# Kernel tuning notes

Measured on AMD Instinct MI355X. Metric: run time of the kernel, lower is better.

Reference implementation:

```python
import jax, jax.numpy as jnp
import numpy as np

B, N, DIM = 2, 4096, 1024
QK = 128
HID = 2048  # int(2.0 * DIM)
EPS = 1e-5


def setup_inputs() -> dict:
    key = jax.random.key(0)
    ks = jax.random.split(key, 10)
    s = lambda fan_in: 1.0 / np.sqrt(fan_in)
    return {
        "x": jax.random.normal(ks[0], (B, N, DIM), dtype=jnp.float32),
        "ln_g": jnp.ones((DIM,), jnp.float32),
        "ln_b": jnp.zeros((DIM,), jnp.float32),
        "Wh": jax.random.uniform(ks[1], (DIM, 2 * HID), jnp.float32, -s(DIM), s(DIM)),
        "bh": jax.random.uniform(ks[2], (2 * HID,), jnp.float32, -s(DIM), s(DIM)),
        "Wqk": jax.random.uniform(ks[3], (DIM, QK), jnp.float32, -s(DIM), s(DIM)),
        "bqk": jax.random.uniform(ks[4], (QK,), jnp.float32, -s(DIM), s(DIM)),
        "gamma": 1.0 + 0.02 * jax.random.normal(ks[5], (2, QK), jnp.float32),
        "beta": jnp.zeros((2, QK), jnp.float32),
        "Wo": jax.random.uniform(ks[6], (HID, DIM), jnp.float32, -s(HID), s(HID)),
        "bo": jax.random.uniform(ks[7], (DIM,), jnp.float32, -s(HID), s(HID)),
    }


def _gau(x, ln_g, ln_b, Wh, bh, Wqk, bqk, gamma, beta, Wo, bo):
    n = x.shape[-2]
    # LayerNorm
    mu = jnp.mean(x, axis=-1, keepdims=True)
    var = jnp.var(x, axis=-1, keepdims=True)
    normed = (x - mu) * jax.lax.rsqrt(var + EPS) * ln_g + ln_b
    # hidden: v and gate
    hv = jax.nn.silu(normed @ Wh + bh)           # [b, n, 2*HID]
    v, gate = hv[..., :HID], hv[..., HID:]
    # q, k via shared projection + offset-scale (2 heads)
    qk = jax.nn.silu(normed @ Wqk + bqk)         # [b, n, QK]
    q = qk * gamma[0] + beta[0]
    k = qk * gamma[1] + beta[1]
    # ReLU^2 attention, scaled by 1/seq_len
    sim = jnp.einsum('bid,bjd->bij', q, k) / n   # [b, n, n]
    attn = jnp.square(jax.nn.relu(sim))
    # causal mask (zero out strict upper triangle)
    causal = jnp.tril(jnp.ones((n, n), dtype=bool))
    attn = jnp.where(causal, attn, 0.0)
    out = jnp.einsum('bij,bjd->bid', attn, v) * gate
    out = out @ Wo + bo
    return out + x  # residual


def reference(x, ln_g, ln_b, Wh, bh, Wqk, bqk, gamma, beta, Wo, bo):
    return _gau(x, ln_g, ln_b, Wh, bh, Wqk, bqk, gamma, beta, Wo, bo)
```

## Files before the change

kernel.cpp:

```cpp
#include <hip/hip_runtime.h>
#include <math.h>

typedef unsigned short u16;
typedef unsigned int u32;
typedef __attribute__((ext_vector_type(8))) __bf16 bf16x8;
typedef __attribute__((ext_vector_type(4))) float f32x4;

#define B_ 2
#define N_ 4096
#define DIM_ 1024
#define QK_ 128
#define HID_ 2048
#define M_TOT (B_*N_)

__device__ __forceinline__ u16 f2bf(float f) {
  union { float f; u32 u; } v; v.f = f;
  u32 r = v.u + 0x7fffu + ((v.u >> 16) & 1u);
  return (u16)(r >> 16);
}
__device__ __forceinline__ float bf2f(u16 h) {
  union { u32 u; float f; } v; v.u = ((u32)h) << 16;
  return v.f;
}
__device__ __forceinline__ float silu_f(float v) { return v / (1.0f + expf(-v)); }

#define WAIT_VM(n)  asm volatile("s_waitcnt vmcnt(" #n ")" ::: "memory")
#define WAIT_LG0()  asm volatile("s_waitcnt lgkmcnt(0)" ::: "memory")

__global__ __launch_bounds__(256) void ln_kernel(
    const float* __restrict__ x, const float* __restrict__ g,
    const float* __restrict__ b, u16* __restrict__ out) {
  const int row = blockIdx.x;
  const int t = threadIdx.x;
  const float4* xr = (const float4*)(x + (size_t)row * DIM_);
  float4 v = xr[t];
  float s  = v.x + v.y + v.z + v.w;
  float s2 = v.x*v.x + v.y*v.y + v.z*v.z + v.w*v.w;
  #pragma unroll
  for (int o = 32; o > 0; o >>= 1) { s += __shfl_down(s, o); s2 += __shfl_down(s2, o); }
  __shared__ float red[2][4];
  const int wave = t >> 6, lane = t & 63;
  if (lane == 0) { red[0][wave] = s; red[1][wave] = s2; }
  __syncthreads();
  float ts  = red[0][0] + red[0][1] + red[0][2] + red[0][3];
  float ts2 = red[1][0] + red[1][1] + red[1][2] + red[1][3];
  float mu  = ts * (1.0f/(float)DIM_);
  float var = ts2 * (1.0f/(float)DIM_) - mu*mu;
  float rs  = rsqrtf(var + 1e-5f);
  const float4 gg = ((const float4*)g)[t];
  const float4 bb = ((const float4*)b)[t];
  ushort4 w;
  w.x = f2bf((v.x-mu)*rs*gg.x + bb.x);
  w.y = f2bf((v.y-mu)*rs*gg.y + bb.y);
  w.z = f2bf((v.z-mu)*rs*gg.z + bb.z);
  w.w = f2bf((v.w-mu)*rs*gg.w + bb.w);
  ((ushort4*)(out + (size_t)row*DIM_))[t] = w;
}

__global__ __launch_bounds__(256) void transpose_k(
    const float* __restrict__ in, u16* __restrict__ out, int R, int C) {
  __shared__ float tile[32][33];
  const int c0 = blockIdx.x * 32, r0 = blockIdx.y * 32;
  const int tx = threadIdx.x & 31, ty = threadIdx.x >> 5;
  #pragma unroll
  for (int i = 0; i < 4; ++i)
    tile[ty + i*8][tx] = in[(size_t)(r0 + ty + i*8) * C + c0 + tx];
  __syncthreads();
  #pragma unroll
  for (int i = 0; i < 4; ++i)
    out[(size_t)(c0 + ty + i*8) * R + r0 + tx] = f2bf(tile[tx][ty + i*8]);
}

enum { EPI_HV, EPI_QK, EPI_S, EPI_PV, EPI_O };

template<int EPI>
__global__ __launch_bounds__(256, 4) void g2(
    const u16* __restrict__ A, int lda,
    const u16* __restrict__ BT, int ldb, int K,
    void* __restrict__ Cv, int ldc,
    const float* __restrict__ f0,
    const u16* __restrict__ gateT, const float* __restrict__ xres)
{
  int bm, bn; const int bz = blockIdx.z;
  bn = blockIdx.x; bm = blockIdx.y;
  if constexpr (EPI == EPI_S) { if (bm < bn) return; }

  const u16* Ap = A; const u16* Bp = BT;
  if constexpr (EPI == EPI_S)  { Ap += (size_t)bz*N_*QK_; Bp += (size_t)bz*N_*QK_; }

  __shared__ __align__(16) u16 lds[2][128*64];
  const int tid = threadIdx.x, wave = tid >> 6, lane = tid & 63;
  const int m0 = bm*128, n0 = bn*128;
  f32x4 acc[4][4] = {};
  const int wr = (wave >> 1)*64, wc = (wave & 1)*64;

  const int srow = lane >> 3;
  const int sch  = (lane & 7) ^ srow;
  const u16* ga = Ap + (size_t)(m0 + srow)*lda + sch*8;
  const u16* gb = Bp + (size_t)(n0 + srow)*ldb + sch*8;

  const int l15   = lane & 15;
  const int cswz0 = ((((lane>>4)    ) ^ (lane&7)) << 3);
  const int cswz1 = ((((lane>>4) | 4) ^ (lane&7)) << 3);

  for (int k0 = 0; k0 < K; k0 += 64) {
    #pragma unroll
    for (int t = 0; t < 4; ++t) {
      const int chunk = wave*4 + t;
      __builtin_amdgcn_global_load_lds(
          (const __attribute__((address_space(1))) void*)(ga + (size_t)(chunk*8)*lda + k0),
          (__attribute__((address_space(3))) void*)&lds[0][chunk*512], 16, 0, 0);
      __builtin_amdgcn_global_load_lds(
          (const __attribute__((address_space(1))) void*)(gb + (size_t)(chunk*8)*ldb + k0),
          (__attribute__((address_space(3))) void*)&lds[1][chunk*512], 16, 0, 0);
    }
    __syncthreads();
    #pragma unroll
    for (int kk = 0; kk < 2; ++kk) {
      const int cs = kk ? cswz1 : cswz0;
      bf16x8 af[4], bfr[4];
      #pragma unroll
      for (int i = 0; i < 4; ++i) {
        af[i]  = *(const bf16x8*)&lds[0][(wr + i*16 + l15)*64 + cs];
        bfr[i] = *(const bf16x8*)&lds[1][(wc + i*16 + l15)*64 + cs];
      }
      #pragma unroll
      for (int i = 0; i < 4; ++i)
        #pragma unroll
        for (int j = 0; j < 4; ++j)
          acc[i][j] = __builtin_amdgcn_mfma_f32_16x16x32_bf16(af[i], bfr[j], acc[i][j], 0, 0, 0);
    }
    __syncthreads();
  }

  const int er = (lane >> 4)*4;
  #pragma unroll
  for (int i = 0; i < 4; ++i) {
    #pragma unroll
    for (int j = 0; j < 4; ++j) {
      #pragma unroll
      for (int e = 0; e < 4; ++e) {
        const int row = m0 + wr + i*16 + er + e;
        const int col = n0 + wc + j*16 + l15;
        float v = acc[i][j][e];
        if constexpr (EPI == EPI_S) {
          float p = (row >= col && v > 0.0f) ? v*v : 0.0f;
          ((u16*)Cv)[(size_t)bz*N_*N_ + (size_t)row*ldc + col] = f2bf(p);
        }
      }
    }
  }
}

template<int BM, int EPI>
__global__ __launch_bounds__(512, 2) void p8(
    const u16* __restrict__ A, int lda,
    const u16* __restrict__ BT, int ldb, int K,
    void* __restrict__ Cv, int ldc,
    const float* __restrict__ f0,
    const u16* __restrict__ gateT, const float* __restrict__ xres)
{
  constexpr int FR  = BM/32;
  constexpr int HF  = FR/2;
  constexpr int ATL = BM*64;
  constexpr int SLT = ATL + 256*64;
  __shared__ __align__(16) u16 lds[2*SLT];

  int bm, bn;
  const int bz = blockIdx.z;
  if constexpr (EPI == EPI_HV) {
    const int id  = (int)blockIdx.x + 16*(int)blockIdx.y;
    const int nid = (id & 7)*64 + (id >> 3);
    bm = nid & 15; bn = nid >> 4;
  } else if constexpr (EPI == EPI_PV) {
    bn = blockIdx.x;
    bm = bz ? ((int)gridDim.y - 1 - (int)blockIdx.y) : (int)blockIdx.y;
  } else { bm = blockIdx.x; bn = blockIdx.y; }

  const int tid = threadIdx.x, wave = tid >> 6, lane = tid & 63;
  const int wm = wave >> 2, wn = wave & 3;
  const int m0 = bm*BM, n0 = bn*256;
  const u16* Ap = A; const u16* Bp = BT;
  if constexpr (EPI == EPI_PV) { Ap += (size_t)bz*N_*N_; Bp += (size_t)bz*N_; }
  int kmax = K;
  if constexpr (EPI == EPI_PV) kmax = (bm+1)*BM;
  const int nt = kmax >> 6;

  const int l15  = lane & 15;
  const int c0   = (((lane>>4)    ) ^ (lane&7)) << 3;
  const int c1   = (((lane>>4) | 4) ^ (lane&7)) << 3;
  const int srow = lane >> 3;
  const int scol = ((lane&7) ^ (lane>>3)) << 3;

  f32x4 acc[FR][4] = {};
  bf16x8 af[HF][2], b0[2][2], b1[2][2];

  auto stage = [&](int slot, int unit, int t) {
    if (t >= nt) return;
    const int k0 = t << 6;
    if (unit == 0 || unit == 3) {
      const int ih = (unit == 3) ? 1 : 0;
      constexpr int LA = BM/128;
      #pragma unroll
      for (int l = 0; l < LA; ++l) {
        const int pa = wave*LA + l;
        const int row0 = (pa/(BM/32))*(BM/2) + ih*(BM/4) + (pa%(BM/32))*8;
        __builtin_amdgcn_global_load_lds(
          (const __attribute__((address_space(1))) void*)(Ap + (size_t)(m0+row0+srow)*lda + k0 + scol),
          (__attribute__((address_space(3))) void*)&lds[slot*SLT + row0*64], 16, 0, 0);
      }
    } else {
      const int jh = (unit == 2) ? 1 : 0;
      #pragma unroll
      for (int l = 0; l < 2; ++l) {
        const int pb = wave*2 + l;
        const int row0 = (pb>>2)*64 + jh*32 + (pb&3)*8;
        __builtin_amdgcn_global_load_lds(
          (const __attribute__((address_space(1))) void*)(Bp + (size_t)(n0+row0+srow)*ldb + k0 + scol),
          (__attribute__((address_space(3))) void*)&lds[slot*SLT + ATL + row0*64], 16, 0, 0);
      }
    }
  };
  auto rdA = [&](int slot, int ih) {
    #pragma unroll
    for (int i = 0; i < HF; ++i) {
      const int R = wm*(BM/2) + ih*(BM/4) + i*16 + l15;
      af[i][0] = *(const bf16x8*)&lds[slot*SLT + R*64 + c0];
      af[i][1] = *(const bf16x8*)&lds[slot*SLT + R*64 + c1];
    }
  };
  auto rdB = [&](int slot, int jh, bf16x8 (&bb)[2][2]) {
    #pragma unroll
    for (int j = 0; j < 2; ++j) {
      const int R = wn*64 + jh*32 + j*16 + l15;
      bb[j][0] = *(const bf16x8*)&lds[slot*SLT + ATL + R*64 + c0];
      bb[j][1] = *(const bf16x8*)&lds[slot*SLT + ATL + R*64 + c1];
    }
  };
  auto mma = [&](int ih, int jh, bf16x8 (&bb)[2][2]) {
    __builtin_amdgcn_s_setprio(1);
    #pragma unroll
    for (int i = 0; i < HF; ++i)
      #pragma unroll
      for (int j = 0; j < 2; ++j)
        #pragma unroll
        for (int kk = 0; kk < 2; ++kk)
          acc[ih*HF+i][jh*2+j] = __builtin_amdgcn_mfma_f32_16x16x32_bf16(
              af[i][kk], bb[j][kk], acc[ih*HF+i][jh*2+j], 0, 0, 0);
    __builtin_amdgcn_s_setprio(0);
  };

  #define BAR()     __builtin_amdgcn_s_barrier()
  #define PH_TAIL() { BAR(); WAIT_LG0(); }
  #define LG8()     if constexpr (BM==256) { asm volatile("s_waitcnt lgkmcnt(8)" ::: "memory"); }

  stage(0,0,0); stage(0,1,0); stage(0,2,0); stage(0,3,0);
  if constexpr (BM==256) { WAIT_VM(4); } else { WAIT_VM(3); }
  stage(1,0,1); stage(1,1,1); stage(1,2,1);
  if constexpr (BM==256) { WAIT_VM(6); } else { WAIT_VM(5); }
  BAR();

  const int iters = nt >> 1;
  for (int it = 0; it < iters; ++it) {
    const int kt = it*2;
    const bool last = (it == iters-1);
    rdA(0,0); rdB(0,0,b0); stage(1,3,kt+1);
    LG8();
    PH_TAIL(); mma(0,0,b0); BAR();
    rdB(0,1,b1); stage(0,0,kt+2);
    PH_TAIL(); mma(0,1,b1); BAR();
    rdA(0,1); stage(0,1,kt+2);
    PH_TAIL(); mma(1,1,b1); BAR();
    stage(0,2,kt+2);
    if (last) { WAIT_VM(0); }
    else if constexpr (BM==256) { WAIT_VM(6); } else { WAIT_VM(5); }
    PH_TAIL(); mma(1,0,b0); BAR();
    rdA(1,0); rdB(1,0,b0); stage(0,3,kt+2);
    LG8();
    PH_TAIL(); mma(0,0,b0); BAR();
    rdB(1,1,b1); stage(1,0,kt+3);
    PH_TAIL(); mma(0,1,b1); BAR();
    rdA(1,1); stage(1,1,kt+3);
    PH_TAIL(); mma(1,1,b1); BAR();
    stage(1,2,kt+3);
    if constexpr (BM==256) { WAIT_VM(6); } else { WAIT_VM(5); }
    PH_TAIL(); mma(1,0,b0); BAR();
  }

  const int er = (lane >> 4)*4;
  #pragma unroll
  for (int fi = 0; fi < FR; ++fi) {
    #pragma unroll
    for (int fj = 0; fj < 4; ++fj) {
      #pragma unroll
      for (int e = 0; e < 4; ++e) {
        const int row = m0 + wm*(BM/2) + fi*16 + er + e;
        const int col = n0 + wn*64 + fj*16 + l15;
        float v = acc[fi][fj][e];
        if constexpr (EPI == EPI_HV) {
          ((u16*)Cv)[(size_t)row*ldc + col] = f2bf(silu_f(v + f0[row]));
        } else if constexpr (EPI == EPI_PV) {
          float gate = bf2f(gateT[(size_t)(HID_ + col)*M_TOT + (size_t)bz*N_ + row]);
          ((u16*)Cv)[((size_t)bz*N_ + row)*ldc + col] = f2bf(v * gate);
        } else {
          ((float*)Cv)[(size_t)row*ldc + col] = v + f0[col] + xres[(size_t)row*DIM_ + col];
        }
      }
    }
  }
  #undef BAR
  #undef PH_TAIL
  #undef LG8
}

template<int BM, int EPI>
__global__ __launch_bounds__(256, 2) void ring4(
    const u16* __restrict__ A, int lda,
    const u16* __restrict__ BT, int ldb, int K,
    void* __restrict__ Cv, void* __restrict__ C2v, int ldc,
    const float* __restrict__ f0, const float* __restrict__ f1,
    const float* __restrict__ f2)
{
  constexpr int FRM  = BM/32;
  constexpr int LA   = BM/64;
  constexpr int ASZ  = BM*32;
  constexpr int SLOT = ASZ + 128*32;
  __shared__ __align__(16) u16 lds[4*SLOT];

  const int bm = blockIdx.x, bn = blockIdx.y;
  const int tid = threadIdx.x, wave = tid >> 6, lane = tid & 63;
  const int wm = wave >> 1, wn = wave & 1;
  const int m0 = bm*BM, n0 = bn*128;
  const int nt = K >> 5;

  f32x4 acc[FRM][4] = {};
  const int srow = lane >> 2;
  const int sq   = (lane & 3) ^ ((srow >> 1) & 3);

  auto stage = [&](int t) {
    if (t >= nt) return;
    const int k0 = t << 5;
    u16* sA = &lds[(t & 3) * SLOT];
    u16* sB = sA + ASZ;
    #pragma unroll
    for (int c = 0; c < LA; ++c) {
      const int ch = wave*LA + c;
      const u16* src = A + (size_t)(m0 + ch*16 + srow)*lda + k0 + sq*8;
      __builtin_amdgcn_global_load_lds(
          (const __attribute__((address_space(1))) void*)src,
          (__attribute__((address_space(3))) void*)(sA + ch*512), 16, 0, 0);
    }
    #pragma unroll
    for (int c = 0; c < 2; ++c) {
      const int ch = wave*2 + c;
      const u16* src = BT + (size_t)(n0 + ch*16 + srow)*ldb + k0 + sq*8;
      __builtin_amdgcn_global_load_lds(
          (const __attribute__((address_space(1))) void*)src,
          (__attribute__((address_space(3))) void*)(sB + ch*512), 16, 0, 0);
    }
  };

  stage(0); stage(1); stage(2);

  const int l15 = lane & 15;
  const int swz = (((lane >> 4) ^ ((l15 >> 1) & 3)) << 3);
  const int rA0 = (wm*(BM/2) + l15)*32;
  const int rB0 = (wn*64 + l15)*32;

  for (int t = 0; t < nt; ++t) {
    if (t + 2 < nt)      { WAIT_VM(8); }
    else if (t + 1 < nt) { WAIT_VM(4); }
    else                 { WAIT_VM(0); }
    __builtin_amdgcn_s_barrier();
    stage(t + 3);

    const u16* sA = &lds[(t & 3) * SLOT];
    const u16* sB = sA + ASZ;
    bf16x8 a_[FRM], b_[4];
    #pragma unroll
    for (int j = 0; j < 4; ++j) b_[j] = *(const bf16x8*)&sB[rB0 + j*512 + swz];
    #pragma unroll
    for (int i = 0; i < FRM; ++i) a_[i] = *(const bf16x8*)&sA[rA0 + i*512 + swz];
    #pragma unroll
    for (int i = 0; i < FRM; ++i)
      #pragma unroll
      for (int j = 0; j < 4; ++j)
        acc[i][j] = __builtin_amdgcn_mfma_f32_16x16x32_bf16(a_[i], b_[j], acc[i][j], 0, 0, 0);
  }

  const int er = (lane >> 4)*4;
  #pragma unroll
  for (int fi = 0; fi < FRM; ++fi) {
    #pragma unroll
    for (int fj = 0; fj < 4; ++fj) {
      #pragma unroll
      for (int e = 0; e < 4; ++e) {
        const int row = m0 + wm*(BM/2) + fi*16 + er + e;
        const int col = n0 + wn*64 + fj*16 + l15;
        float v = acc[fi][fj][e];
        if constexpr (EPI == EPI_QK) {
          float s = silu_f(v + f0[col]);
          float q = (s*f1[col]     + f2[col])     * (1.0f/(float)N_);
          float k2 = s*f1[QK_+col] + f2[QK_+col];
          ((u16*)Cv )[(size_t)row*ldc + col] = f2bf(q);
          ((u16*)C2v)[(size_t)row*ldc + col] = f2bf(k2);
        }
      }
    }
  }
}

extern "C" void kernel_launch(void* const* d_in, const int* in_sizes, int n_in,
                              void* d_out, int out_size, void* d_ws, size_t ws_size,
                              hipStream_t stream) {
  const float* x    = (const float*)d_in[0];
  const float* ln_g = (const float*)d_in[1];
  const float* ln_b = (const float*)d_in[2];
  const float* Wh   = (const float*)d_in[3];
  const float* bh   = (const float*)d_in[4];
  const float* Wqk  = (const float*)d_in[5];
  const float* bqk  = (const float*)d_in[6];
  const float* gamma= (const float*)d_in[7];
  const float* beta = (const float*)d_in[8];
  const float* Wo   = (const float*)d_in[9];
  const float* bo   = (const float*)d_in[10];
  float* out = (float*)d_out;
  char* ws = (char*)d_ws;

  u16* normed = (u16*)(ws + 0);
  u16* WhT    = (u16*)(ws + 16777216);
  u16* WqkT   = (u16*)(ws + 25165824);
  u16* WoT    = (u16*)(ws + 25427968);
  u16* hvT    = (u16*)(ws + 29622272);
  u16* qs     = (u16*)(ws + 96731136);
  u16* kb     = (u16*)(ws + 98828288);
  u16* P      = (u16*)(ws + 100925440);
  u16* a2     = (u16*)(ws + 168034304);

  ln_kernel<<<M_TOT, 256, 0, stream>>>(x, ln_g, ln_b, normed);
  transpose_k<<<dim3(4096/32, 1024/32), 256, 0, stream>>>(Wh,  WhT,  1024, 4096);
  transpose_k<<<dim3( 128/32, 1024/32), 256, 0, stream>>>(Wqk, WqkT, 1024, 128);
  transpose_k<<<dim3(1024/32, 2048/32), 256, 0, stream>>>(Wo,  WoT,  2048, 1024);

  p8<256, EPI_HV><<<dim3(16, 32), 512, 0, stream>>>(WhT, 1024, normed, 1024, 1024,
      hvT, 8192, bh, nullptr, nullptr);
  ring4<64, EPI_QK><<<dim3(128, 1), 256, 0, stream>>>(normed, 1024, WqkT, 1024, 1024,
      qs, kb, 128, bqk, gamma, beta);
  g2<EPI_S><<<dim3(32, 32, 2), 256, 0, stream>>>(qs, 128, kb, 128, 128,
      P, 4096, nullptr, nullptr, nullptr);
  p8<128, EPI_PV><<<dim3(8, 32, 2), 512, 0, stream>>>(P, 4096, hvT, 8192, 4096,
      a2, 2048, nullptr, hvT, nullptr);
  p8<128, EPI_O><<<dim3(64, 4), 512, 0, stream>>>(a2, 2048, WoT, 2048, 2048,
      out, 1024, bo, nullptr, x);
}
```

Baseline: 266.4 us.

## Swap GEMM kernels: HV projection on g2 tiles, score GEMM on ring4 pipeline

The hidden projection GEMM (4096x8192x1024) now runs on the simpler 128x128 double-buffered g2 kernel with a grouped block-index swizzle, instead of the 256-row p8 kernel. The causal score GEMM (K=128) moves from g2 to ring4, which has a 4-slot LDS ring with a tuned vmcnt wait schedule that scales with loads per thread. The aim is to match each kernel's tiling and pipelining to its GEMM's shape. The risk is lower per-tile data reuse and different occupancy for the large HV GEMM.

```diff
diff --git a/kernel.cpp b/kernel.cpp
--- a/kernel.cpp
+++ b/kernel.cpp
@@ -78,15 +78,14 @@
     const u16* __restrict__ A, int lda,
     const u16* __restrict__ BT, int ldb, int K,
     void* __restrict__ Cv, int ldc,
-    const float* __restrict__ f0,
-    const u16* __restrict__ gateT, const float* __restrict__ xres)
+    const float* __restrict__ f0)
 {
-  int bm, bn; const int bz = blockIdx.z;
-  bn = blockIdx.x; bm = blockIdx.y;
-  if constexpr (EPI == EPI_S) { if (bm < bn) return; }
-
-  const u16* Ap = A; const u16* Bp = BT;
-  if constexpr (EPI == EPI_S)  { Ap += (size_t)bz*N_*QK_; Bp += (size_t)bz*N_*QK_; }
+  int bm, bn;
+  {
+    const int id  = (int)blockIdx.x + 32*(int)blockIdx.y;
+    const int nid = (id & 7)*256 + (id >> 3);
+    bm = nid & 31; bn = nid >> 5;
+  }
 
   __shared__ __align__(16) u16 lds[2][128*64];
   const int tid = threadIdx.x, wave = tid >> 6, lane = tid & 63;
@@ -96,8 +95,8 @@
 
   const int srow = lane >> 3;
   const int sch  = (lane & 7) ^ srow;
-  const u16* ga = Ap + (size_t)(m0 + srow)*lda + sch*8;
-  const u16* gb = Bp + (size_t)(n0 + srow)*ldb + sch*8;
+  const u16* ga = A  + (size_t)(m0 + srow)*lda + sch*8;
+  const u16* gb = BT + (size_t)(n0 + srow)*ldb + sch*8;
 
   const int l15   = lane & 15;
   const int cswz0 = ((((lane>>4)    ) ^ (lane&7)) << 3);
@@ -143,7 +142,114 @@
         const int row = m0 + wr + i*16 + er + e;
         const int col = n0 + wc + j*16 + l15;
         float v = acc[i][j][e];
-        if constexpr (EPI == EPI_S) {
+        ((u16*)Cv)[(size_t)row*ldc + col] = f2bf(silu_f(v + f0[row]));
+      }
+    }
+  }
+}
+
+template<int BM, int EPI>
+__global__ __launch_bounds__(256, 2) void ring4(
+    const u16* __restrict__ A, int lda,
+    const u16* __restrict__ BT, int ldb, int K,
+    void* __restrict__ Cv, void* __restrict__ C2v, int ldc,
+    const float* __restrict__ f0, const float* __restrict__ f1,
+    const float* __restrict__ f2)
+{
+  constexpr int FRM  = BM/32;
+  constexpr int LA   = BM/64;
+  constexpr int LPT  = LA + 2;
+  constexpr int ASZ  = BM*32;
+  constexpr int SLOT = ASZ + 128*32;
+  __shared__ __align__(16) u16 lds[4*SLOT];
+
+  int bm, bn;
+  const int bz = blockIdx.z;
+  if constexpr (EPI == EPI_S) {
+    bn = blockIdx.x; bm = blockIdx.y;
+    if (bm < bn) return;
+  } else { bm = blockIdx.x; bn = blockIdx.y; }
+
+  const u16* Ap = A; const u16* Bp = BT;
+  if constexpr (EPI == EPI_S) { Ap += (size_t)bz*N_*QK_; Bp += (size_t)bz*N_*QK_; }
+
+  const int tid = threadIdx.x, wave = tid >> 6, lane = tid & 63;
+  const int wm = wave >> 1, wn = wave & 1;
+  const int m0 = bm*BM, n0 = bn*128;
+  const int nt = K >> 5;
+
+  f32x4 acc[FRM][4] = {};
+  const int srow = lane >> 2;
+  const int sq   = (lane & 3) ^ ((srow >> 1) & 3);
+
+  auto stage = [&](int t) {
+    if (t >= nt) return;
+    const int k0 = t << 5;
+    u16* sA = &lds[(t & 3) * SLOT];
+    u16* sB = sA + ASZ;
+    #pragma unroll
+    for (int c = 0; c < LA; ++c) {
+      const int ch = wave*LA + c;
+      const u16* src = Ap + (size_t)(m0 + ch*16 + srow)*lda + k0 + sq*8;
+      __builtin_amdgcn_global_load_lds(
+          (const __attribute__((address_space(1))) void*)src,
+          (__attribute__((address_space(3))) void*)(sA + ch*512), 16, 0, 0);
+    }
+    #pragma unroll
+    for (int c = 0; c < 2; ++c) {
+      const int ch = wave*2 + c;
+      const u16* src = Bp + (size_t)(n0 + ch*16 + srow)*ldb + k0 + sq*8;
+      __builtin_amdgcn_global_load_lds(
+          (const __attribute__((address_space(1))) void*)src,
+          (__attribute__((address_space(3))) void*)(sB + ch*512), 16, 0, 0);
+    }
+  };
+
+  stage(0); stage(1); stage(2);
+
+  const int l15 = lane & 15;
+  const int swz = (((lane >> 4) ^ ((l15 >> 1) & 3)) << 3);
+  const int rA0 = (wm*(BM/2) + l15)*32;
+  const int rB0 = (wn*64 + l15)*32;
+
+  for (int t = 0; t < nt; ++t) {
+    if (t + 2 < nt)      { if constexpr (LPT==4) { WAIT_VM(8); } else { WAIT_VM(6); } }
+    else if (t + 1 < nt) { if constexpr (LPT==4) { WAIT_VM(4); } else { WAIT_VM(3); } }
+    else                 { WAIT_VM(0); }
+    __builtin_amdgcn_s_barrier();
+    stage(t + 3);
+
+    const u16* sA = &lds[(t & 3) * SLOT];
+    const u16* sB = sA + ASZ;
+    bf16x8 a_[FRM], b_[4];
+    #pragma unroll
+    for (int j = 0; j < 4; ++j) b_[j] = *(const bf16x8*)&sB[rB0 + j*512 + swz];
+    #pragma unroll
+    for (int i = 0; i < FRM; ++i) a_[i] = *(const bf16x8*)&sA[rA0 + i*512 + swz];
+    #pragma unroll
+    for (int i = 0; i < FRM; ++i)
+      #pragma unroll
+      for (int j = 0; j < 4; ++j)
+        acc[i][j] = __builtin_amdgcn_mfma_f32_16x16x32_bf16(a_[i], b_[j], acc[i][j], 0, 0, 0);
+  }
+
+  const int er = (lane >> 4)*4;
+  #pragma unroll
+  for (int fi = 0; fi < FRM; ++fi) {
+    #pragma unroll
+    for (int fj = 0; fj < 4; ++fj) {
+      #pragma unroll
+      for (int e = 0; e < 4; ++e) {
+        const int row = m0 + wm*(BM/2) + fi*16 + er + e;
+        const int col = n0 + wn*64 + fj*16 + l15;
+        float v = acc[fi][fj][e];
+        if constexpr (EPI == EPI_QK) {
+          float s = silu_f(v + f0[col]);
+          float q = (s*f1[col]     + f2[col])     * (1.0f/(float)N_);
+          float k2 = s*f1[QK_+col] + f2[QK_+col];
+          ((u16*)Cv )[(size_t)row*ldc + col] = f2bf(q);
+          ((u16*)C2v)[(size_t)row*ldc + col] = f2bf(k2);
+        } else if constexpr (EPI == EPI_S) {
           float p = (row >= col && v > 0.0f) ? v*v : 0.0f;
           ((u16*)Cv)[(size_t)bz*N_*N_ + (size_t)row*ldc + col] = f2bf(p);
         }
@@ -168,11 +274,7 @@
 
   int bm, bn;
   const int bz = blockIdx.z;
-  if constexpr (EPI == EPI_HV) {
-    const int id  = (int)blockIdx.x + 16*(int)blockIdx.y;
-    const int nid = (id & 7)*64 + (id >> 3);
-    bm = nid & 15; bn = nid >> 4;
-  } else if constexpr (EPI == EPI_PV) {
+  if constexpr (EPI == EPI_PV) {
     bn = blockIdx.x;
     bm = bz ? ((int)gridDim.y - 1 - (int)blockIdx.y) : (int)blockIdx.y;
   } else { bm = blockIdx.x; bn = blockIdx.y; }
@@ -297,9 +399,7 @@
         const int row = m0 + wm*(BM/2) + fi*16 + er + e;
         const int col = n0 + wn*64 + fj*16 + l15;
         float v = acc[fi][fj][e];
-        if constexpr (EPI == EPI_HV) {
-          ((u16*)Cv)[(size_t)row*ldc + col] = f2bf(silu_f(v + f0[row]));
-        } else if constexpr (EPI == EPI_PV) {
+        if constexpr (EPI == EPI_PV) {
           float gate = bf2f(gateT[(size_t)(HID_ + col)*M_TOT + (size_t)bz*N_ + row]);
           ((u16*)Cv)[((size_t)bz*N_ + row)*ldc + col] = f2bf(v * gate);
         } else {
@@ -311,103 +411,6 @@
   #undef BAR
   #undef PH_TAIL
   #undef LG8
-}
-
-template<int BM, int EPI>
-__global__ __launch_bounds__(256, 2) void ring4(
-    const u16* __restrict__ A, int lda,
-    const u16* __restrict__ BT, int ldb, int K,
-    void* __restrict__ Cv, void* __restrict__ C2v, int ldc,
-    const float* __restrict__ f0, const float* __restrict__ f1,
-    const float* __restrict__ f2)
-{
-  constexpr int FRM  = BM/32;
-  constexpr int LA   = BM/64;
-  constexpr int ASZ  = BM*32;
-  constexpr int SLOT = ASZ + 128*32;
-  __shared__ __align__(16) u16 lds[4*SLOT];
-
-  const int bm = blockIdx.x, bn = blockIdx.y;
-  const int tid = threadIdx.x, wave = tid >> 6, lane = tid & 63;
-  const int wm = wave >> 1, wn = wave & 1;
-  const int m0 = bm*BM, n0 = bn*128;
-  const int nt = K >> 5;
-
-  f32x4 acc[FRM][4] = {};
-  const int srow = lane >> 2;
-  const int sq   = (lane & 3) ^ ((srow >> 1) & 3);
-
-  auto stage = [&](int t) {
-    if (t >= nt) return;
-    const int k0 = t << 5;
-    u16* sA = &lds[(t & 3) * SLOT];
-    u16* sB = sA + ASZ;
-    #pragma unroll
-    for (int c = 0; c < LA; ++c) {
-      const int ch = wave*LA + c;
-      const u16* src = A + (size_t)(m0 + ch*16 + srow)*lda + k0 + sq*8;
-      __builtin_amdgcn_global_load_lds(
-          (const __attribute__((address_space(1))) void*)src,
-          (__attribute__((address_space(3))) void*)(sA + ch*512), 16, 0, 0);
-    }
-    #pragma unroll
-    for (int c = 0; c < 2; ++c) {
-      const int ch = wave*2 + c;
-      const u16* src = BT + (size_t)(n0 + ch*16 + srow)*ldb + k0 + sq*8;
-      __builtin_amdgcn_global_load_lds(
-          (const __attribute__((address_space(1))) void*)src,
-          (__attribute__((address_space(3))) void*)(sB + ch*512), 16, 0, 0);
-    }
-  };
-
-  stage(0); stage(1); stage(2);
-
-  const int l15 = lane & 15;
-  const int swz = (((lane >> 4) ^ ((l15 >> 1) & 3)) << 3);
-  const int rA0 = (wm*(BM/2) + l15)*32;
-  const int rB0 = (wn*64 + l15)*32;
-
-  for (int t = 0; t < nt; ++t) {
-    if (t + 2 < nt)      { WAIT_VM(8); }
-    else if (t + 1 < nt) { WAIT_VM(4); }
-    else                 { WAIT_VM(0); }
-    __builtin_amdgcn_s_barrier();
-    stage(t + 3);
-
-    const u16* sA = &lds[(t & 3) * SLOT];
-    const u16* sB = sA + ASZ;
-    bf16x8 a_[FRM], b_[4];
-    #pragma unroll
-    for (int j = 0; j < 4; ++j) b_[j] = *(const bf16x8*)&sB[rB0 + j*512 + swz];
-    #pragma unroll
-    for (int i = 0; i < FRM; ++i) a_[i] = *(const bf16x8*)&sA[rA0 + i*512 + swz];
-    #pragma unroll
-    for (int i = 0; i < FRM; ++i)
-      #pragma unroll
-      for (int j = 0; j < 4; ++j)
-        acc[i][j] = __builtin_amdgcn_mfma_f32_16x16x32_bf16(a_[i], b_[j], acc[i][j], 0, 0, 0);
-  }
-
-  const int er = (lane >> 4)*4;
-  #pragma unroll
-  for (int fi = 0; fi < FRM; ++fi) {
-    #pragma unroll
-    for (int fj = 0; fj < 4; ++fj) {
-      #pragma unroll
-      for (int e = 0; e < 4; ++e) {
-        const int row = m0 + wm*(BM/2) + fi*16 + er + e;
-        const int col = n0 + wn*64 + fj*16 + l15;
-        float v = acc[fi][fj][e];
-        if constexpr (EPI == EPI_QK) {
-          float s = silu_f(v + f0[col]);
-          float q = (s*f1[col]     + f2[col])     * (1.0f/(float)N_);
-          float k2 = s*f1[QK_+col] + f2[QK_+col];
-          ((u16*)Cv )[(size_t)row*ldc + col] = f2bf(q);
-          ((u16*)C2v)[(size_t)row*ldc + col] = f2bf(k2);
-        }
-      }
-    }
-  }
 }
 
 extern "C" void kernel_launch(void* const* d_in, const int* in_sizes, int n_in,
@@ -442,12 +445,12 @@
   transpose_k<<<dim3( 128/32, 1024/32), 256, 0, stream>>>(Wqk, WqkT, 1024, 128);
   transpose_k<<<dim3(1024/32, 2048/32), 256, 0, stream>>>(Wo,  WoT,  2048, 1024);
 
-  p8<256, EPI_HV><<<dim3(16, 32), 512, 0, stream>>>(WhT, 1024, normed, 1024, 1024,
-      hvT, 8192, bh, nullptr, nullptr);
+  g2<EPI_HV><<<dim3(32, 64), 256, 0, stream>>>(WhT, 1024, normed, 1024, 1024,
+      hvT, 8192, bh);
   ring4<64, EPI_QK><<<dim3(128, 1), 256, 0, stream>>>(normed, 1024, WqkT, 1024, 1024,
       qs, kb, 128, bqk, gamma, beta);
-  g2<EPI_S><<<dim3(32, 32, 2), 256, 0, stream>>>(qs, 128, kb, 128, 128,
-      P, 4096, nullptr, nullptr, nullptr);
+  ring4<128, EPI_S><<<dim3(32, 32, 2), 256, 0, stream>>>(qs, 128, kb, 128, 128,
+      P, nullptr, 4096, nullptr, nullptr, nullptr);
   p8<128, EPI_PV><<<dim3(8, 32, 2), 512, 0, stream>>>(P, 4096, hvT, 8192, 4096,
       a2, 2048, nullptr, hvT, nullptr);
   p8<128, EPI_O><<<dim3(64, 4), 512, 0, stream>>>(a2, 2048, WoT, 2048, 2048,
```

Measured after the change: 280.3 us. +5.2%, slower.
